# Kernel tuning notes

Hardware: AMD Instinct MI355X
Metric: run time of the kernel (lower is better)

The kernel has to match this reference:

```python
import jax, jax.numpy as jnp
import numpy as np

NODES = [2048, 4096, 8192]
LAMB = 0.5  # sparsity penalty, applied only at layer 0


def tanh_deriv(x):
    t = jnp.tanh(x)
    return 1.0 - t * t


def setup_inputs() -> dict:
    key = jax.random.key(0)
    k1, k2, k3, k4 = jax.random.split(key, 4)
    B = 256
    batch_inp = jax.random.normal(k1, (B, NODES[2]), jnp.float32)
    # torch Linear weight layout: (out_features, in_features)
    W0 = jax.random.normal(k2, (NODES[1], NODES[0]), jnp.float32) / np.float32(np.sqrt(NODES[0]))
    W1 = jax.random.normal(k3, (NODES[2], NODES[1]), jnp.float32) / np.float32(np.sqrt(NODES[1]))
    memory = jax.random.normal(k4, (NODES[0],), jnp.float32) * 0.1
    return {"batch_inp": batch_inp, "W0": W0, "W1": W1, "memory": memory,
            "n_iters": 8, "inf_lr": 0.05}


def reference(batch_inp, W0, W1, memory, n_iters, inf_lr):
    B = batch_inp.shape[0]
    inf_lr = jnp.float32(inf_lr)

    def compute_errs(v0, v1, v2):
        # update_err_nodes: e_l = v_l - pred_l
        e0 = v0 - memory
        e1 = v1 - jnp.tanh(v0) @ W0.T   # [B, n1]
        e2 = v2 - jnp.tanh(v1) @ W1.T   # [B, n2]
        return e0, e1, e2

    def energy(e0, e1, e2):
        return (jnp.sum(e0 * e0) + jnp.sum(e1 * e1) + jnp.sum(e2 * e2)) * (100.0 / B)

    # set_nodes: v0 = memory (broadcast over batch -- identical to torch broadcasting),
    # v1 = forward prediction, v2 clamped to input.
    v0 = jnp.broadcast_to(memory, (B, NODES[0]))
    v1 = jnp.tanh(v0) @ W0.T
    v2 = batch_inp
    e0, e1, e2 = compute_errs(v0, v1, v2)

    def step(carry, _):
        v0, v1, e0, e1, e2 = carry
        # update_val_nodes (torch.no_grad block): all errs are pre-update values
        d0 = -e0 - LAMB * jnp.sign(v0) + tanh_deriv(v0) * (e1 @ W0)
        nv0 = jax.lax.stop_gradient(jax.nn.relu(v0 + inf_lr * d0))
        d1 = -e1 + tanh_deriv(v1) * (e2 @ W1)
        nv1 = jax.lax.stop_gradient(jax.nn.relu(v1 + inf_lr * d1))
        ne0, ne1, ne2 = compute_errs(nv0, nv1, v2)
        return (nv0, nv1, ne0, ne1, ne2), energy(ne0, ne1, ne2)

    _, losses = jax.lax.scan(step, (v0, v1, e0, e1, e2), None, length=n_iters)
    return losses  # [n_iters] per-iteration energies (inf_losses)
```

## Files before the change

kernel.cpp:

```cpp
#include <hip/hip_runtime.h>
#include <hip/hip_bf16.h>
#include <stdint.h>


typedef short short8x __attribute__((ext_vector_type(8)));
typedef float float4x __attribute__((ext_vector_type(4)));
typedef unsigned short u16;
typedef u16 u16x8 __attribute__((ext_vector_type(8)));

static constexpr float LOSS_SCALE = 100.0f / 256.0f;

__device__ __forceinline__ u16 f2b(float x) {
    union { float f; uint32_t u; } v{x};
    uint32_t b = v.u + 0x7fffu + ((v.u >> 16) & 1u);
    return (u16)(b >> 16);
}

__device__ __forceinline__ float signf_(float x) {
    return (x > 0.f) ? 1.f : ((x < 0.f) ? -1.f : 0.f);
}

__device__ __forceinline__ void gload_lds16(const void* g, void* lds) {
    __builtin_amdgcn_global_load_lds(
        (const __attribute__((address_space(1))) void*)g,
        (__attribute__((address_space(3))) void*)lds, 16, 0, 0);
}

__global__ void k_zero(float* p, int n) {
    int i = blockIdx.x * blockDim.x + threadIdx.x;
    if (i < n) p[i] = 0.f;
}

__global__ __launch_bounds__(256) void k_cast_both(
    const float* __restrict__ in, u16* __restrict__ outN, u16* __restrict__ outT,
    int R, int C) {
    __shared__ float tile[32][33];
    int x = blockIdx.x * 32 + threadIdx.x;
#pragma unroll
    for (int k = 0; k < 32; k += 8) {
        int y = blockIdx.y * 32 + threadIdx.y + k;
        float v = in[(size_t)y * C + x];
        tile[threadIdx.y + k][threadIdx.x] = v;
        outN[(size_t)y * C + x] = f2b(v);
    }
    __syncthreads();
    int ox = blockIdx.y * 32 + threadIdx.x;
#pragma unroll
    for (int k = 0; k < 32; k += 8) {
        int oy = blockIdx.x * 32 + threadIdx.y + k;
        outT[(size_t)oy * R + ox] = f2b(tile[threadIdx.x][threadIdx.y + k]);
    }
}

__global__ void k_fill_v0(float* __restrict__ v0, const float* __restrict__ memory,
                          int n, int mask) {
    int i = blockIdx.x * blockDim.x + threadIdx.x;
    if (i < n) v0[i] = memory[i & mask];
}

__global__ void k_tanh(float* __restrict__ dst, const float* __restrict__ src, int n) {
    int i = blockIdx.x * blockDim.x + threadIdx.x;
    if (i < n) dst[i] = tanhf(src[i]);
}

__global__ void k_rowdot(const float* __restrict__ x, const float* __restrict__ W,
                         float* __restrict__ out, int K) {
    int i = blockIdx.x;
    const float* w = W + (size_t)i * K;
    float s = 0.f;
    for (int j = threadIdx.x; j < K; j += 256) s += x[j] * w[j];
    __shared__ float red[256];
    red[threadIdx.x] = s;
    __syncthreads();
    for (int st = 128; st > 0; st >>= 1) {
        if (threadIdx.x < st) red[threadIdx.x] += red[threadIdx.x + st];
        __syncthreads();
    }
    if (threadIdx.x == 0) out[i] = red[0];
}

__global__ void k_bcast_v1_e1(float* __restrict__ v1, float* __restrict__ e1,
                              u16* __restrict__ e1b,
                              const float* __restrict__ r1, int n, int mask) {
    int i = blockIdx.x * blockDim.x + threadIdx.x;
    if (i < n) { v1[i] = r1[i & mask]; e1[i] = 0.f; e1b[i] = 0; }
}

__global__ void k_e2_init(u16* __restrict__ e2b, const float* __restrict__ inp,
                          const float* __restrict__ r2, int n, int mask) {
    int i = blockIdx.x * blockDim.x + threadIdx.x;
    if (i < n) e2b[i] = f2b(inp[i] - r2[i & mask]);
}

struct GGR {
    const u16* A;
    const u16* Bt;
    float* Cp;
    int N, K, nCol, ks;
};

__device__ void gemm_part(const GGR& g, int t, u16* stage) {
    const int tid = threadIdx.x;
    const int w = tid >> 6, l = tid & 63;
    const int lm = l & 15, lq = l >> 4;
    const int cb = t / g.ks, kq = t - cb * g.ks;
    const int K = g.K;
    const int Ksl = K / g.ks;
    const int nCh = Ksl >> 5;
    const int col0 = cb * 64;

    u16* base = stage + (w << 13);
    const u16* aSrc = g.A + (size_t)(w * 64 + (l >> 2)) * K + kq * Ksl + (l & 3) * 8;
    const u16* bSrc = g.Bt + (size_t)(col0 + (l >> 2)) * K + kq * Ksl + (l & 3) * 8;
    const size_t rStep = (size_t)16 * K;

    int aoff[4];
#pragma unroll
    for (int i = 0; i < 4; ++i) aoff[i] = (i * 16 + lm) * 32 + lq * 8;

    float4x acc[4][4];
#pragma unroll
    for (int i = 0; i < 4; ++i)
#pragma unroll
        for (int j = 0; j < 4; ++j) acc[i][j] = (float4x)0.f;

#define ISSUE(c, b) { \
    u16* ab = base + (b) * 4096; \
    const u16* as = aSrc + (c) * 32; \
    const u16* bs = bSrc + (c) * 32; \
    gload_lds16(as, ab);             gload_lds16(as + rStep, ab + 512); \
    gload_lds16(as + 2*rStep, ab + 1024); gload_lds16(as + 3*rStep, ab + 1536); \
    gload_lds16(bs, ab + 2048);      gload_lds16(bs + rStep, ab + 2560); \
    gload_lds16(bs + 2*rStep, ab + 3072); gload_lds16(bs + 3*rStep, ab + 3584); }

#define COMPUTE(b) { \
    u16* ab = base + (b) * 4096; \
    short8x a[4], bb[4]; \
    _Pragma("unroll") for (int i = 0; i < 4; ++i) a[i] = *(const short8x*)(ab + aoff[i]); \
    _Pragma("unroll") for (int j = 0; j < 4; ++j) bb[j] = *(const short8x*)(ab + 2048 + aoff[j]); \
    _Pragma("unroll") for (int i = 0; i < 4; ++i) \
    _Pragma("unroll") for (int j = 0; j < 4; ++j) \
        acc[i][j] = __builtin_amdgcn_mfma_f32_16x16x32_bf16(a[i], bb[j], acc[i][j], 0, 0, 0); }

    ISSUE(0, 0);
    int c = 0;
    for (; c < nCh - 1; ++c) {
        __builtin_amdgcn_sched_barrier(0);
        ISSUE(c + 1, (c + 1) & 1);
        __builtin_amdgcn_sched_barrier(0);
        __builtin_amdgcn_s_waitcnt(0x0F78);
        __builtin_amdgcn_sched_barrier(0);
        COMPUTE(c & 1);
    }
    __builtin_amdgcn_sched_barrier(0);
    __builtin_amdgcn_s_waitcnt(0x0F70);
    __builtin_amdgcn_sched_barrier(0);
    COMPUTE(c & 1);
#undef ISSUE
#undef COMPUTE

    float* cp = g.Cp + ((size_t)(kq * 256 + w * 64) * g.N + col0);
#pragma unroll
    for (int i = 0; i < 4; ++i)
#pragma unroll
        for (int j = 0; j < 4; ++j)
#pragma unroll
            for (int r = 0; r < 4; ++r)
                cp[(size_t)(i * 16 + lq * 4 + r) * g.N + j * 16 + lm] = acc[i][j][r];
}

__global__ __launch_bounds__(256, 2) void pcn_gemm(GGR ga, GGR gb, int nA) {
    __shared__ u16 stage[32768];
    int bx = blockIdx.x;
    if (bx < nA) gemm_part(ga, bx, stage);
    else         gemm_part(gb, bx - nA, stage);
}

struct EGR {
    const float* P;
    const float* x0;
    const float* x1;
    float* y0;
    u16* y0b;
    u16* y1b;
    float* loss;
    const float* lr;
    int N, nCol, ks;
};

template <int EPI>
__device__ void epi_tile(const EGR& g, int tile, float* red8) {
    const int t = threadIdx.x;
    const int w = t >> 6, l = t & 63;
    const int rowBlk = tile / g.nCol, colBlk = tile - rowBlk * g.nCol;
    const int row0 = rowBlk * 64, col0 = colBlk * 64;
    const int row = t >> 3, c8 = (t & 7) * 8;
    const size_t idx = (size_t)(row0 + row) * g.N + col0 + c8;
    const size_t plane = (size_t)256 * g.N;

    const float* p0 = g.P + idx;
    float4x cv[2];
    cv[0] = *(const float4x*)(p0);
    cv[1] = *(const float4x*)(p0 + 4);
    for (int q = 1; q < g.ks; ++q) {
        cv[0] += *(const float4x*)(p0 + (size_t)q * plane);
        cv[1] += *(const float4x*)(p0 + (size_t)q * plane + 4);
    }

    float lr = 0.f;
    if (EPI == 1 || EPI == 2) lr = *g.lr;
    float lsum = 0.f;

    if (EPI == 1) {
        float4x vv[2], mm[2], nv[2]; u16x8 tb;
        vv[0] = *(const float4x*)(g.x0 + idx);       vv[1] = *(const float4x*)(g.x0 + idx + 4);
        mm[0] = *(const float4x*)(g.x1 + col0 + c8); mm[1] = *(const float4x*)(g.x1 + col0 + c8 + 4);
#pragma unroll
        for (int h = 0; h < 2; ++h)
#pragma unroll
            for (int e = 0; e < 4; ++e) {
                float v = vv[h][e], th = tanhf(v), td = 1.f - th * th;
                float d0 = (mm[h][e] - v) - 0.5f * signf_(v) + td * cv[h][e];
                float x = v + lr * d0;
                x = x > 0.f ? x : 0.f;
                nv[h][e] = x;
                tb[h * 4 + e] = f2b(tanhf(x));
                float ne0 = x - mm[h][e];
                lsum += ne0 * ne0;
            }
        *(float4x*)(g.y0 + idx) = nv[0];
        *(float4x*)(g.y0 + idx + 4) = nv[1];
        *(u16x8*)(g.y1b + idx) = tb;
    } else if (EPI == 2) {
        float4x vv[2], ee[2], nv[2]; u16x8 tb;
        vv[0] = *(const float4x*)(g.x0 + idx);     vv[1] = *(const float4x*)(g.x0 + idx + 4);
        ee[0] = *(const float4x*)(g.x1 + idx);     ee[1] = *(const float4x*)(g.x1 + idx + 4);
#pragma unroll
        for (int h = 0; h < 2; ++h)
#pragma unroll
            for (int e = 0; e < 4; ++e) {
                float v = vv[h][e], th = tanhf(v), td = 1.f - th * th;
                float x = v + lr * (-ee[h][e] + td * cv[h][e]);
                x = x > 0.f ? x : 0.f;
                nv[h][e] = x;
                tb[h * 4 + e] = f2b(tanhf(x));
            }
        *(float4x*)(g.y0 + idx) = nv[0];
        *(float4x*)(g.y0 + idx + 4) = nv[1];
        *(u16x8*)(g.y1b + idx) = tb;
    } else if (EPI == 3) {
        float4x vv[2], ne[2]; u16x8 nb;
        vv[0] = *(const float4x*)(g.x0 + idx);     vv[1] = *(const float4x*)(g.x0 + idx + 4);
#pragma unroll
        for (int h = 0; h < 2; ++h)
#pragma unroll
            for (int e = 0; e < 4; ++e) {
                float x = vv[h][e] - cv[h][e];
                ne[h][e] = x;
                nb[h * 4 + e] = f2b(x);
                lsum += x * x;
            }
        *(float4x*)(g.y0 + idx) = ne[0];
        *(float4x*)(g.y0 + idx + 4) = ne[1];
        *(u16x8*)(g.y0b + idx) = nb;
    } else {
        float4x vv[2]; u16x8 nb;
        vv[0] = *(const float4x*)(g.x0 + idx);     vv[1] = *(const float4x*)(g.x0 + idx + 4);
#pragma unroll
        for (int h = 0; h < 2; ++h)
#pragma unroll
            for (int e = 0; e < 4; ++e) {
                float x = vv[h][e] - cv[h][e];
                nb[h * 4 + e] = f2b(x);
                lsum += x * x;
            }
        *(u16x8*)(g.y1b + idx) = nb;
    }

    if (EPI != 2) {
#pragma unroll
        for (int off = 32; off > 0; off >>= 1) lsum += __shfl_down(lsum, off);
        if (l == 0) red8[w] = lsum;
        __syncthreads();
        if (t == 0) {
            float s = 0.f;
#pragma unroll
            for (int q = 0; q < 8; ++q) s += red8[q];
            atomicAdd(g.loss, s * LOSS_SCALE);
        }
    }
}

template <int EPIA, int EPIB>
__global__ __launch_bounds__(512) void pcn_epi(EGR ga, EGR gb, int nA) {
    __shared__ float red8[8];
    int bx = blockIdx.x;
    if (bx < nA) epi_tile<EPIA>(ga, bx, red8);
    else         epi_tile<EPIB>(gb, bx - nA, red8);
}

extern "C" void kernel_launch(void* const* d_in, const int* in_sizes, int n_in,
                              void* d_out, int out_size, void* d_ws, size_t ws_size,
                              hipStream_t stream)
{
    const float* batch_inp = (const float*)d_in[0];
    const float* W0        = (const float*)d_in[1];
    const float* W1        = (const float*)d_in[2];
    const float* memory    = (const float*)d_in[3];
    const float* lr_ptr    = (const float*)d_in[5];
    float* out = (float*)d_out;

    const int n0 = 2048, n1 = 4096, n2 = 8192, Bn = 256;

    char* ws = (char*)d_ws;
    auto alloc_f = [&](size_t n) { float* p = (float*)ws; ws += n * 4; return p; };
    auto alloc_b = [&](size_t n) { u16* p = (u16*)ws; ws += n * 2; return p; };

    float* v0  = alloc_f((size_t)Bn * n0);
    float* v1  = alloc_f((size_t)Bn * n1);
    float* e1  = alloc_f((size_t)Bn * n1);
    u16*   e1b = alloc_b((size_t)Bn * n1);
    u16*   e2b = alloc_b((size_t)Bn * n2);
    u16*   T0b = alloc_b((size_t)Bn * n0);
    u16*   T1b = alloc_b((size_t)Bn * n1);
    u16*   W0b  = alloc_b((size_t)n1 * n0);
    u16*   W0Tb = alloc_b((size_t)n0 * n1);
    u16*   W1b  = alloc_b((size_t)n2 * n1);
    u16*   W1Tb = alloc_b((size_t)n1 * n2);
    float* tm = alloc_f(n0);
    float* r1 = alloc_f(n1);
    float* t1 = alloc_f(n1);
    float* r2 = alloc_f(n2);
    float* CpA = alloc_f((size_t)8 * Bn * n1);
    float* CpB = alloc_f((size_t)4 * Bn * n0);

    k_zero<<<1, 32, 0, stream>>>(out, 8);
    k_cast_both<<<dim3(n0 / 32, n1 / 32), dim3(32, 8), 0, stream>>>(W0, W0b, W0Tb, n1, n0);
    k_cast_both<<<dim3(n1 / 32, n2 / 32), dim3(32, 8), 0, stream>>>(W1, W1b, W1Tb, n2, n1);
    k_fill_v0<<<(Bn * n0) / 256, 256, 0, stream>>>(v0, memory, Bn * n0, n0 - 1);
    k_tanh<<<n0 / 256, 256, 0, stream>>>(tm, memory, n0);
    k_rowdot<<<n1, 256, 0, stream>>>(tm, W0, r1, n0);
    k_tanh<<<n1 / 256, 256, 0, stream>>>(t1, r1, n1);
    k_bcast_v1_e1<<<(Bn * n1) / 256, 256, 0, stream>>>(v1, e1, e1b, r1, Bn * n1, n1 - 1);
    k_rowdot<<<n2, 256, 0, stream>>>(t1, W1, r2, n1);
    k_e2_init<<<(Bn * n2) / 256, 256, 0, stream>>>(e2b, batch_inp, r2, Bn * n2, n2 - 1);

    for (int it = 0; it < 8; ++it) {
        float* loss = out + it;

        GGR g2{e2b, W1Tb, CpA, n1, n2, n1 / 64, 8};
        GGR g1{e1b, W0Tb, CpB, n0, n1, n0 / 64, 4};
        pcn_gemm<<<(n1 / 64) * 8 + (n0 / 64) * 4, 256, 0, stream>>>(g2, g1, (n1 / 64) * 8);

        EGR e2g{CpA, v1, e1, v1, nullptr, T1b, nullptr, lr_ptr, n1, n1 / 64, 8};
        EGR e1g{CpB, v0, memory, v0, nullptr, T0b, loss, lr_ptr, n0, n0 / 64, 4};
        pcn_epi<2, 1><<<4 * (n1 / 64) + 4 * (n0 / 64), 512, 0, stream>>>(
            e2g, e1g, 4 * (n1 / 64));

        GGR g4{T1b, W1b, CpA, n2, n1, n2 / 64, 4};
        GGR g3{T0b, W0b, CpB, n1, n0, n1 / 64, 2};
        pcn_gemm<<<(n2 / 64) * 4 + (n1 / 64) * 2, 256, 0, stream>>>(g4, g3, (n2 / 64) * 4);

        EGR e4g{CpA, batch_inp, nullptr, nullptr, nullptr, e2b, loss, nullptr, n2, n2 / 64, 4};
        EGR e3g{CpB, v1, nullptr, e1, e1b, nullptr, loss, nullptr, n1, n1 / 64, 2};
        pcn_epi<4, 3><<<4 * (n2 / 64) + 4 * (n1 / 64), 512, 0, stream>>>(
            e4g, e3g, 4 * (n2 / 64));
    }
}
```

Baseline: 1.303 ms.

## Widen GEMM tiles to 256x128 with shared B, triple-buffered staging, higher split-K

The split-K GEMM changes from per-wave private 64x64 tiles to a block-shared 256x128 tile. The four waves now cooperatively stage one shared 128-column B slab, and staging moves to a three-buffer global-to-LDS pipeline with workgroup barriers. Split-K factors are raised, doubling when the workspace is large enough, so grid size stays up despite the wider column tiles. The weight cast kernel uses 64x64 tiles and the rowdot setup uses float4 loads. In exchange, each thread holds twice as many accumulators (register pressure), adds barrier synchronisation, and writes more partial planes that the epilogue must reduce.

```diff
diff --git a/kernel.cpp b/kernel.cpp
--- a/kernel.cpp
+++ b/kernel.cpp
@@ -34,20 +34,20 @@
 __global__ __launch_bounds__(256) void k_cast_both(
     const float* __restrict__ in, u16* __restrict__ outN, u16* __restrict__ outT,
     int R, int C) {
-    __shared__ float tile[32][33];
-    int x = blockIdx.x * 32 + threadIdx.x;
-#pragma unroll
-    for (int k = 0; k < 32; k += 8) {
-        int y = blockIdx.y * 32 + threadIdx.y + k;
+    __shared__ float tile[64][65];
+    int x = blockIdx.x * 64 + threadIdx.x;
+#pragma unroll
+    for (int k = 0; k < 64; k += 4) {
+        int y = blockIdx.y * 64 + threadIdx.y + k;
         float v = in[(size_t)y * C + x];
         tile[threadIdx.y + k][threadIdx.x] = v;
         outN[(size_t)y * C + x] = f2b(v);
     }
     __syncthreads();
-    int ox = blockIdx.y * 32 + threadIdx.x;
-#pragma unroll
-    for (int k = 0; k < 32; k += 8) {
-        int oy = blockIdx.x * 32 + threadIdx.y + k;
+    int ox = blockIdx.y * 64 + threadIdx.x;
+#pragma unroll
+    for (int k = 0; k < 64; k += 4) {
+        int oy = blockIdx.x * 64 + threadIdx.y + k;
         outT[(size_t)oy * R + ox] = f2b(tile[threadIdx.x][threadIdx.y + k]);
     }
 }
@@ -66,9 +66,13 @@
 __global__ void k_rowdot(const float* __restrict__ x, const float* __restrict__ W,
                          float* __restrict__ out, int K) {
     int i = blockIdx.x;
-    const float* w = W + (size_t)i * K;
+    const float4* w = (const float4*)(W + (size_t)i * K);
+    const float4* xv = (const float4*)x;
     float s = 0.f;
-    for (int j = threadIdx.x; j < K; j += 256) s += x[j] * w[j];
+    for (int j = threadIdx.x; j < (K >> 2); j += 256) {
+        float4 a = xv[j], b = w[j];
+        s += a.x * b.x + a.y * b.y + a.z * b.z + a.w * b.w;
+    }
     __shared__ float red[256];
     red[threadIdx.x] = s;
     __syncthreads();
@@ -99,78 +103,83 @@
     int N, K, nCol, ks;
 };
 
-__device__ void gemm_part(const GGR& g, int t, u16* stage) {
+__device__ void gemm_part(const GGR& g, int bx, u16* stage) {
     const int tid = threadIdx.x;
     const int w = tid >> 6, l = tid & 63;
     const int lm = l & 15, lq = l >> 4;
-    const int cb = t / g.ks, kq = t - cb * g.ks;
+    const int cb = bx / g.ks, kq = bx - cb * g.ks;
     const int K = g.K;
     const int Ksl = K / g.ks;
     const int nCh = Ksl >> 5;
-    const int col0 = cb * 64;
-
-    u16* base = stage + (w << 13);
+
     const u16* aSrc = g.A + (size_t)(w * 64 + (l >> 2)) * K + kq * Ksl + (l & 3) * 8;
-    const u16* bSrc = g.Bt + (size_t)(col0 + (l >> 2)) * K + kq * Ksl + (l & 3) * 8;
+    const u16* bSrc = g.Bt + (size_t)(cb * 128 + w * 32 + (l >> 2)) * K + kq * Ksl + (l & 3) * 8;
     const size_t rStep = (size_t)16 * K;
 
-    int aoff[4];
-#pragma unroll
-    for (int i = 0; i < 4; ++i) aoff[i] = (i * 16 + lm) * 32 + lq * 8;
-
-    float4x acc[4][4];
+    int aoff[4], boff[8];
+#pragma unroll
+    for (int i = 0; i < 4; ++i) aoff[i] = w * 2048 + i * 512 + lm * 32 + lq * 8;
+#pragma unroll
+    for (int j = 0; j < 8; ++j) boff[j] = 8192 + j * 512 + lm * 32 + lq * 8;
+
+    float4x acc[4][8];
 #pragma unroll
     for (int i = 0; i < 4; ++i)
 #pragma unroll
-        for (int j = 0; j < 4; ++j) acc[i][j] = (float4x)0.f;
-
-#define ISSUE(c, b) { \
-    u16* ab = base + (b) * 4096; \
+        for (int j = 0; j < 8; ++j) acc[i][j] = (float4x)0.f;
+
+#define STAGE(c, bf) { \
+    u16* ad = stage + (bf) * 12288 + w * 2048; \
+    u16* bd = stage + (bf) * 12288 + 8192 + w * 1024; \
     const u16* as = aSrc + (c) * 32; \
     const u16* bs = bSrc + (c) * 32; \
-    gload_lds16(as, ab);             gload_lds16(as + rStep, ab + 512); \
-    gload_lds16(as + 2*rStep, ab + 1024); gload_lds16(as + 3*rStep, ab + 1536); \
-    gload_lds16(bs, ab + 2048);      gload_lds16(bs + rStep, ab + 2560); \
-    gload_lds16(bs + 2*rStep, ab + 3072); gload_lds16(bs + 3*rStep, ab + 3584); }
-
-#define COMPUTE(b) { \
-    u16* ab = base + (b) * 4096; \
-    short8x a[4], bb[4]; \
+    gload_lds16(as, ad);                  gload_lds16(as + rStep, ad + 512); \
+    gload_lds16(as + 2 * rStep, ad + 1024); gload_lds16(as + 3 * rStep, ad + 1536); \
+    gload_lds16(bs, bd);                  gload_lds16(bs + rStep, bd + 512); }
+
+#define COMPUTE(bf) { \
+    u16* ab = stage + (bf) * 12288; \
+    short8x a[4], bb[8]; \
     _Pragma("unroll") for (int i = 0; i < 4; ++i) a[i] = *(const short8x*)(ab + aoff[i]); \
-    _Pragma("unroll") for (int j = 0; j < 4; ++j) bb[j] = *(const short8x*)(ab + 2048 + aoff[j]); \
+    _Pragma("unroll") for (int j = 0; j < 8; ++j) bb[j] = *(const short8x*)(ab + boff[j]); \
     _Pragma("unroll") for (int i = 0; i < 4; ++i) \
-    _Pragma("unroll") for (int j = 0; j < 4; ++j) \
+    _Pragma("unroll") for (int j = 0; j < 8; ++j) \
         acc[i][j] = __builtin_amdgcn_mfma_f32_16x16x32_bf16(a[i], bb[j], acc[i][j], 0, 0, 0); }
 
-    ISSUE(0, 0);
-    int c = 0;
-    for (; c < nCh - 1; ++c) {
-        __builtin_amdgcn_sched_barrier(0);
-        ISSUE(c + 1, (c + 1) & 1);
-        __builtin_amdgcn_sched_barrier(0);
-        __builtin_amdgcn_s_waitcnt(0x0F78);
-        __builtin_amdgcn_sched_barrier(0);
-        COMPUTE(c & 1);
-    }
-    __builtin_amdgcn_sched_barrier(0);
-    __builtin_amdgcn_s_waitcnt(0x0F70);
-    __builtin_amdgcn_sched_barrier(0);
-    COMPUTE(c & 1);
-#undef ISSUE
+    STAGE(0, 0);
+    STAGE(1, 1);
+    int bf = 0, sf = 2;
+    for (int c = 0; c < nCh; ++c) {
+        __builtin_amdgcn_sched_barrier(0);
+        if (c + 2 < nCh) { STAGE(c + 2, sf); }
+        __builtin_amdgcn_sched_barrier(0);
+        if (c + 2 < nCh)      __builtin_amdgcn_s_waitcnt(0x0F7C);
+        else if (c + 1 < nCh) __builtin_amdgcn_s_waitcnt(0x0F76);
+        else                  __builtin_amdgcn_s_waitcnt(0x0F70);
+        __builtin_amdgcn_sched_barrier(0);
+        __builtin_amdgcn_s_barrier();
+        __builtin_amdgcn_sched_barrier(0);
+        COMPUTE(bf);
+        __builtin_amdgcn_sched_barrier(0);
+        __builtin_amdgcn_s_barrier();
+        bf = (bf == 2) ? 0 : bf + 1;
+        sf = (sf == 2) ? 0 : sf + 1;
+    }
+#undef STAGE
 #undef COMPUTE
 
-    float* cp = g.Cp + ((size_t)(kq * 256 + w * 64) * g.N + col0);
+    float* cp = g.Cp + ((size_t)kq * 256 + w * 64) * g.N + (size_t)cb * 128;
 #pragma unroll
     for (int i = 0; i < 4; ++i)
 #pragma unroll
-        for (int j = 0; j < 4; ++j)
+        for (int j = 0; j < 8; ++j)
 #pragma unroll
             for (int r = 0; r < 4; ++r)
                 cp[(size_t)(i * 16 + lq * 4 + r) * g.N + j * 16 + lm] = acc[i][j][r];
 }
 
 __global__ __launch_bounds__(256, 2) void pcn_gemm(GGR ga, GGR gb, int nA) {
-    __shared__ u16 stage[32768];
+    __shared__ u16 stage[36864];
     int bx = blockIdx.x;
     if (bx < nA) gemm_part(ga, bx, stage);
     else         gemm_part(gb, bx - nA, stage);
@@ -312,6 +321,13 @@
 
     const int n0 = 2048, n1 = 4096, n2 = 8192, Bn = 256;
 
+    const bool big = ws_size >= (size_t)261 * 1024 * 1024;
+    const int ks2 = big ? 16 : 8;
+    const int ks1 = 8;
+    const int ks4 = big ? 8 : 4;
+    const int ks3 = 4;
+    const int planesA = big ? 16 : 8;
+
     char* ws = (char*)d_ws;
     auto alloc_f = [&](size_t n) { float* p = (float*)ws; ws += n * 4; return p; };
     auto alloc_b = [&](size_t n) { u16* p = (u16*)ws; ws += n * 2; return p; };
@@ -331,12 +347,12 @@
     float* r1 = alloc_f(n1);
     float* t1 = alloc_f(n1);
     float* r2 = alloc_f(n2);
-    float* CpA = alloc_f((size_t)8 * Bn * n1);
-    float* CpB = alloc_f((size_t)4 * Bn * n0);
+    float* CpA = alloc_f((size_t)planesA * Bn * n1);
+    float* CpB = alloc_f((size_t)8 * Bn * n0);
 
     k_zero<<<1, 32, 0, stream>>>(out, 8);
-    k_cast_both<<<dim3(n0 / 32, n1 / 32), dim3(32, 8), 0, stream>>>(W0, W0b, W0Tb, n1, n0);
-    k_cast_both<<<dim3(n1 / 32, n2 / 32), dim3(32, 8), 0, stream>>>(W1, W1b, W1Tb, n2, n1);
+    k_cast_both<<<dim3(n0 / 64, n1 / 64), dim3(64, 4), 0, stream>>>(W0, W0b, W0Tb, n1, n0);
+    k_cast_both<<<dim3(n1 / 64, n2 / 64), dim3(64, 4), 0, stream>>>(W1, W1b, W1Tb, n2, n1);
     k_fill_v0<<<(Bn * n0) / 256, 256, 0, stream>>>(v0, memory, Bn * n0, n0 - 1);
     k_tanh<<<n0 / 256, 256, 0, stream>>>(tm, memory, n0);
     k_rowdot<<<n1, 256, 0, stream>>>(tm, W0, r1, n0);
@@ -348,21 +364,23 @@
     for (int it = 0; it < 8; ++it) {
         float* loss = out + it;
 
-        GGR g2{e2b, W1Tb, CpA, n1, n2, n1 / 64, 8};
-        GGR g1{e1b, W0Tb, CpB, n0, n1, n0 / 64, 4};
-        pcn_gemm<<<(n1 / 64) * 8 + (n0 / 64) * 4, 256, 0, stream>>>(g2, g1, (n1 / 64) * 8);
-
-        EGR e2g{CpA, v1, e1, v1, nullptr, T1b, nullptr, lr_ptr, n1, n1 / 64, 8};
-        EGR e1g{CpB, v0, memory, v0, nullptr, T0b, loss, lr_ptr, n0, n0 / 64, 4};
+        GGR g2{e2b, W1Tb, CpA, n1, n2, n1 / 128, ks2};
+        GGR g1{e1b, W0Tb, CpB, n0, n1, n0 / 128, ks1};
+        pcn_gemm<<<(n1 / 128) * ks2 + (n0 / 128) * ks1, 256, 0, stream>>>(
+            g2, g1, (n1 / 128) * ks2);
+
+        EGR e2g{CpA, v1, e1, v1, nullptr, T1b, nullptr, lr_ptr, n1, n1 / 64, ks2};
+        EGR e1g{CpB, v0, memory, v0, nullptr, T0b, loss, lr_ptr, n0, n0 / 64, ks1};
         pcn_epi<2, 1><<<4 * (n1 / 64) + 4 * (n0 / 64), 512, 0, stream>>>(
             e2g, e1g, 4 * (n1 / 64));
 
-        GGR g4{T1b, W1b, CpA, n2, n1, n2 / 64, 4};
-        GGR g3{T0b, W0b, CpB, n1, n0, n1 / 64, 2};
-        pcn_gemm<<<(n2 / 64) * 4 + (n1 / 64) * 2, 256, 0, stream>>>(g4, g3, (n2 / 64) * 4);
-
-        EGR e4g{CpA, batch_inp, nullptr, nullptr, nullptr, e2b, loss, nullptr, n2, n2 / 64, 4};
-        EGR e3g{CpB, v1, nullptr, e1, e1b, nullptr, loss, nullptr, n1, n1 / 64, 2};
+        GGR g4{T1b, W1b, CpA, n2, n1, n2 / 128, ks4};
+        GGR g3{T0b, W0b, CpB, n1, n0, n1 / 128, ks3};
+        pcn_gemm<<<(n2 / 128) * ks4 + (n1 / 128) * ks3, 256, 0, stream>>>(
+            g4, g3, (n2 / 128) * ks4);
+
+        EGR e4g{CpA, batch_inp, nullptr, nullptr, nullptr, e2b, loss, nullptr, n2, n2 / 64, ks4};
+        EGR e3g{CpB, v1, nullptr, e1, e1b, nullptr, loss, nullptr, n1, n1 / 64, ks3};
         pcn_epi<4, 3><<<4 * (n2 / 64) + 4 * (n1 / 64), 512, 0, stream>>>(
             e4g, e3g, 4 * (n2 / 64));
     }
```

Result: no change. 1.315 ms (+0.9%).
